# Optimization experiments

Hardware: AMD Instinct MI355X
Metric: run time of the kernel (lower is better)

Reference implementation:

```python
import jax, jax.numpy as jnp
import numpy as np

INF = 1000000000000.0
HEAD_SIZE = 64
HEADS = 12
MAX_LENGTH = 512


def _rope_tables(dim, max_length):
    inv_freq = 1.0 / (10000.0 ** (jnp.arange(0, dim, 2, dtype=jnp.float32) / dim))
    t = jnp.arange(max_length, dtype=jnp.float32)
    freqs = t[:, None] * inv_freq[None, :]  # [L, dim/2]
    return jnp.sin(freqs), jnp.cos(freqs)


def _apply_rope(t, sin, cos):
    # t: [B, L, d]; sin/cos: [L, d/2]
    t1, t2 = t[..., 0::2], t[..., 1::2]
    out = jnp.stack([t1 * cos - t2 * sin, t1 * sin + t2 * cos], axis=-1)
    return out.reshape(t.shape)


def setup_inputs() -> dict:
    key = jax.random.key(0)
    k1, k2, k3, k4, k5 = jax.random.split(key, 5)
    B, L, H = 16, 512, 1024
    inputs = jax.random.normal(k1, (B, L, H), dtype=jnp.float32)
    attention_mask = jnp.ones((B, L), dtype=jnp.float32)
    s1 = 1.0 / np.sqrt(H)
    s2 = 1.0 / np.sqrt(HEAD_SIZE * 2)
    W1 = jax.random.normal(k2, (H, HEAD_SIZE * 2), dtype=jnp.float32) * s1
    b1 = jax.random.normal(k3, (HEAD_SIZE * 2,), dtype=jnp.float32) * s1
    W2 = jax.random.normal(k4, (HEAD_SIZE * 2, HEADS * 2), dtype=jnp.float32) * s2
    b2 = jax.random.normal(k5, (HEADS * 2,), dtype=jnp.float32) * s2
    return {"inputs": inputs, "attention_mask": attention_mask,
            "W1": W1, "b1": b1, "W2": W2, "b2": b2}


def reference(inputs, attention_mask, W1, b1, W2, b2):
    B, L, _ = inputs.shape
    x = inputs @ W1 + b1                      # [B, L, 2*head_size]
    qw, kw = x[..., 0::2], x[..., 1::2]        # [B, L, head_size] each
    sin, cos = _rope_tables(HEAD_SIZE, MAX_LENGTH)
    sin, cos = sin[:L], cos[:L]
    qw = _apply_rope(qw, sin, cos)
    kw = _apply_rope(kw, sin, cos)
    logits = jnp.einsum('bmd,bnd->bmn', qw, kw) / (HEAD_SIZE ** 0.5)  # [B, L, L]
    bias = jnp.swapaxes(x @ W2 + b2, 1, 2) / 2.0                       # [B, 2*heads, L]
    # logits[b,h,m,n] = score[b,m,n] + bias_even[b,h,n] + bias_odd[b,h,m]
    logits = logits[:, None] + bias[:, 0::2, None, :] + bias[:, 1::2, :, None]
    attn_mask = 1.0 - attention_mask[:, None, None, :] * attention_mask[:, None, :, None]
    logits = logits - attn_mask * INF
    tril = jnp.tril(jnp.ones((L, L), dtype=logits.dtype), k=-1)
    logits = logits - tril * INF
    return logits
```

## Files before the change

kernel.cpp:

```cpp
#include <hip/hip_runtime.h>
#include <hip/hip_bf16.h>

typedef short bf16x8 __attribute__((ext_vector_type(8)));
typedef float f32x4 __attribute__((ext_vector_type(4)));
typedef unsigned short u16;
typedef unsigned short u16x4 __attribute__((ext_vector_type(4)));
typedef unsigned short u16x8 __attribute__((ext_vector_type(8)));

#define FINF 1.0e12f

__device__ __forceinline__ u16 f2b(float f) {
  union { float f; unsigned int u; } x; x.f = f;
  unsigned int r = x.u + 0x7fffu + ((x.u >> 16) & 1u);
  return (u16)(r >> 16);
}

__global__ __launch_bounds__(256) void k0_w1frag(const float* __restrict__ W1,
                                                 u16* __restrict__ w1f) {
  int t8 = blockIdx.x * 256 + threadIdx.x;
  int ln = t8 & 15;
  int kg = (t8 >> 4) & 3;
  int ksnt = (t8 >> 6) & 15;
  int chunk = t8 >> 10;
  int ks = ksnt & 1, nt = ksnt >> 1;
  int kbase = chunk * 64 + ks * 32 + kg * 8;
  int c = nt * 16 + ln;
  u16x8 v;
  #pragma unroll
  for (int i = 0; i < 8; ++i) v[i] = f2b(W1[(size_t)(kbase + i) * 128 + c]);
  *(u16x8*)&w1f[t8 * 8] = v;
}

__global__ __launch_bounds__(256) void k1_prep(
    const float* __restrict__ inputs, const u16* __restrict__ w1f,
    const float* __restrict__ b1, const float* __restrict__ W2,
    const float* __restrict__ b2,
    u16* __restrict__ qw, u16* __restrict__ kw,
    float* __restrict__ biasE, float* __restrict__ biasO) {
  __shared__ __align__(16) char smem[49536];
  float* w2t = (float*)(smem + 36864);
  float* xt  = (float*)smem;

  int t = threadIdx.x;
  int lane = t & 63, w = t >> 6;
  int r0 = blockIdx.x * 16;
  int b = r0 >> 9, l0 = r0 & 511;

  #pragma unroll
  for (int i = 0; i < 12; ++i) {
    int idx = t + i * 256;
    int k = idx / 24, c = idx - k * 24;
    w2t[c * 132 + k] = W2[idx];
  }

  f32x4 acc[2];
  acc[0] = (f32x4){0.f, 0.f, 0.f, 0.f};
  acc[1] = (f32x4){0.f, 0.f, 0.f, 0.f};

  int wnt = w * 2;

  int arow_s = t >> 4;
  int aseg = t & 15;
  const float* ain = &inputs[(size_t)(r0 + arow_s) * 1024 + aseg * 4];
  int abyt = (arow_s * 128 + aseg * 8) ^ ((arow_s & 7) << 4);
  const float4* wsrcAll = (const float4*)w1f;

  float4 a0 = *(const float4*)(ain);
  float4 wr0 = wsrcAll[t];
  float4 wr1 = wsrcAll[t + 256];
  float4 wr2 = wsrcAll[t + 512];
  float4 wr3 = wsrcAll[t + 768];
  {
    u16x4 av;
    av[0] = f2b(a0.x); av[1] = f2b(a0.y); av[2] = f2b(a0.z); av[3] = f2b(a0.w);
    *(u16x4*)(smem + abyt) = av;
    float4* wd = (float4*)(smem + 4096);
    wd[t] = wr0; wd[t + 256] = wr1; wd[t + 512] = wr2; wd[t + 768] = wr3;
  }
  __syncthreads();

  for (int ch = 0; ch < 16; ++ch) {
    if (ch < 15) {
      a0 = *(const float4*)(ain + (ch + 1) * 64);
      const float4* wsrc = wsrcAll + (ch + 1) * 1024;
      wr0 = wsrc[t]; wr1 = wsrc[t + 256]; wr2 = wsrc[t + 512]; wr3 = wsrc[t + 768];
    }
    {
      const char* Ab = smem + (ch & 1) * 2048;
      const u16* Wb = (const u16*)(smem + 4096 + (ch & 1) * 16384);
      int arow = lane & 15;
      int hi = lane >> 4;
      #pragma unroll
      for (int ks = 0; ks < 2; ++ks) {
        int cb = ks * 64 + hi * 16;
        bf16x8 a = *(const bf16x8*)(Ab + ((arow * 128 + cb) ^ ((arow & 7) << 4)));
        #pragma unroll
        for (int nti = 0; nti < 2; ++nti) {
          int nt = wnt + nti;
          bf16x8 bb = *(const bf16x8*)&Wb[((nt * 2 + ks) * 64 + lane) * 8];
          acc[nti] = __builtin_amdgcn_mfma_f32_16x16x32_bf16(a, bb, acc[nti], 0, 0, 0);
        }
      }
    }
    if (ch < 15) {
      int q = (ch + 1) & 1;
      u16x4 av;
      av[0] = f2b(a0.x); av[1] = f2b(a0.y); av[2] = f2b(a0.z); av[3] = f2b(a0.w);
      *(u16x4*)(smem + q * 2048 + abyt) = av;
      float4* wd = (float4*)(smem + 4096 + q * 16384);
      wd[t] = wr0; wd[t + 256] = wr1; wd[t + 512] = wr2; wd[t + 768] = wr3;
    }
    __syncthreads();
  }
  __syncthreads();

  #pragma unroll
  for (int nti = 0; nti < 2; ++nti) {
    int c = (wnt + nti) * 16 + (lane & 15);
    float b1v = b1[c];
    #pragma unroll
    for (int r = 0; r < 4; ++r) {
      int row = ((lane >> 4) << 2) + r;
      xt[row * 132 + c] = acc[nti][r] + b1v;
    }
  }
  __syncthreads();

  {
    int r = t >> 4, jb = (t & 15) * 2;
    int l = l0 + r;
    float fl = (float)l;
    u16x4 qv, kv;
    #pragma unroll
    for (int p = 0; p < 2; ++p) {
      int j = jb + p;
      float4 x4 = *(const float4*)&xt[r * 132 + 4 * j];
      float invf = exp2f(-0.4152410118609203f * (float)j);
      float ang = fl * invf;
      float rev = ang * 0.15915494309189535f;
      rev = rev - floorf(rev);
      float sv, cv;
      __sincosf(rev * 6.2831853071795864f, &sv, &cv);
      qv[2 * p] = f2b(x4.x * cv - x4.z * sv);
      qv[2 * p + 1] = f2b(x4.x * sv + x4.z * cv);
      kv[2 * p] = f2b(x4.y * cv - x4.w * sv);
      kv[2 * p + 1] = f2b(x4.y * sv + x4.w * cv);
    }
    size_t base = ((size_t)(b * 512 + l)) * 64 + jb * 2;
    *(u16x4*)&qw[base] = qv;
    *(u16x4*)&kw[base] = kv;
  }

  if (t < 192) {
    int c = t >> 3;
    int rg = (t & 7) * 2;
    float s0 = b2[c], s1 = s0;
    #pragma unroll
    for (int k4 = 0; k4 < 32; ++k4) {
      float4 wv = *(const float4*)&w2t[c * 132 + k4 * 4];
      float4 x0 = *(const float4*)&xt[(rg + 0) * 132 + k4 * 4];
      float4 x1 = *(const float4*)&xt[(rg + 1) * 132 + k4 * 4];
      s0 += x0.x * wv.x + x0.y * wv.y + x0.z * wv.z + x0.w * wv.w;
      s1 += x1.x * wv.x + x1.y * wv.y + x1.z * wv.z + x1.w * wv.w;
    }
    int h = c >> 1;
    size_t o = ((size_t)(b * 12 + h)) * 512 + l0 + rg;
    float2 sv = {s0 * 0.5f, s1 * 0.5f};
    if (c & 1) *(float2*)&biasO[o] = sv;
    else       *(float2*)&biasE[o] = sv;
  }
}

__global__ __launch_bounds__(256) void k2_main(
    const u16* __restrict__ qw, const u16* __restrict__ kw,
    const float* __restrict__ biasE, const float* __restrict__ biasO,
    const float* __restrict__ amask, float* __restrict__ out) {
  __shared__ char smem[24448];
  u16* Q = (u16*)smem;
  u16* K = (u16*)(smem + 8192);
  float* qkL = (float*)smem;
  float* BN = (float*)(smem + 17408);
  float* BM = (float*)(smem + 17408 + 3264);
  float* AMm = (float*)(smem + 17408 + 6528);
  float* AMn = AMm + 64;

  int t = threadIdx.x;
  int lane = t & 63, w = t >> 6;
  int n0 = blockIdx.x * 64, m0 = blockIdx.y * 64, b = blockIdx.z;
  bool skip = (m0 >= n0 + 64);

  if (!skip) {
    int row = t >> 2, sg = t & 3;
    const u16x8* qsrc = (const u16x8*)&qw[((size_t)(b * 512 + m0 + row)) * 64 + sg * 16];
    u16x8 q0 = qsrc[0], q1 = qsrc[1];
    const u16x8* ksrc = (const u16x8*)&kw[((size_t)(b * 512 + n0 + row)) * 64 + sg * 16];
    u16x8 k0v = ksrc[0], k1v = ksrc[1];
    int swz = (row & 7) << 4;
    int byt = row * 128 + sg * 32;
    *(u16x8*)((char*)Q + ((byt) ^ swz)) = q0;
    *(u16x8*)((char*)Q + ((byt + 16) ^ swz)) = q1;
    *(u16x8*)((char*)K + ((byt) ^ swz)) = k0v;
    *(u16x8*)((char*)K + ((byt + 16) ^ swz)) = k1v;
  }
  if (t < 192) {
    int h = t >> 4, kq = t & 15;
    *(float4*)&BN[h * 68 + kq * 4] =
        *(const float4*)&biasE[((size_t)(b * 12 + h)) * 512 + n0 + kq * 4];
    *(float4*)&BM[h * 68 + kq * 4] =
        *(const float4*)&biasO[((size_t)(b * 12 + h)) * 512 + m0 + kq * 4];
  } else if (t < 224) {
    int i = t - 192;
    if (i < 16) *(float4*)&AMm[i * 4] = *(const float4*)&amask[b * 512 + m0 + i * 4];
    else { int ii = i - 16; *(float4*)&AMn[ii * 4] = *(const float4*)&amask[b * 512 + n0 + ii * 4]; }
  }
  __syncthreads();

  if (!skip) {
    f32x4 acc[4];
    #pragma unroll
    for (int nt = 0; nt < 4; ++nt) acc[nt] = (f32x4){0.f, 0.f, 0.f, 0.f};
    int mrow = w * 16 + (lane & 15);
    int hi = lane >> 4;
    #pragma unroll
    for (int ks = 0; ks < 2; ++ks) {
      int cb = ks * 64 + hi * 16;
      bf16x8 a = *(const bf16x8*)((const char*)Q +
                                  ((mrow * 128 + cb) ^ ((mrow & 7) << 4)));
      #pragma unroll
      for (int nt = 0; nt < 4; ++nt) {
        int nr = nt * 16 + (lane & 15);
        bf16x8 bb = *(const bf16x8*)((const char*)K +
                                     ((nr * 128 + cb) ^ ((nr & 7) << 4)));
        acc[nt] = __builtin_amdgcn_mfma_f32_16x16x32_bf16(a, bb, acc[nt], 0, 0, 0);
      }
    }
    __syncthreads();
    #pragma unroll
    for (int nt = 0; nt < 4; ++nt)
      #pragma unroll
      for (int r = 0; r < 4; ++r)
        qkL[(w * 16 + hi * 4 + r) * 68 + nt * 16 + (lane & 15)] = acc[nt][r];
    __syncthreads();
  }

  int a15 = t & 15, mb = t >> 4;
  float amn0 = AMn[a15 * 4 + 0], amn1 = AMn[a15 * 4 + 1];
  float amn2 = AMn[a15 * 4 + 2], amn3 = AMn[a15 * 4 + 3];
  float vals[4][4];
  #pragma unroll
  for (int mi = 0; mi < 4; ++mi) {
    int m = mb + 16 * mi;
    int mg = m0 + m;
    float amm = AMm[m];
    int ng = n0 + a15 * 4;
    float p0 = (1.f - amm * amn0) * FINF + ((mg > ng + 0) ? FINF : 0.f);
    float p1 = (1.f - amm * amn1) * FINF + ((mg > ng + 1) ? FINF : 0.f);
    float p2 = (1.f - amm * amn2) * FINF + ((mg > ng + 2) ? FINF : 0.f);
    float p3 = (1.f - amm * amn3) * FINF + ((mg > ng + 3) ? FINF : 0.f);
    if (!skip) {
      float4 qk = *(const float4*)&qkL[m * 68 + a15 * 4];
      vals[mi][0] = qk.x * 0.125f - p0;
      vals[mi][1] = qk.y * 0.125f - p1;
      vals[mi][2] = qk.z * 0.125f - p2;
      vals[mi][3] = qk.w * 0.125f - p3;
    } else {
      vals[mi][0] = -p0; vals[mi][1] = -p1; vals[mi][2] = -p2; vals[mi][3] = -p3;
    }
  }

  size_t outbase = (size_t)(b * 12) * 262144 + (size_t)m0 * 512 + n0 + a15 * 4;
  #pragma unroll
  for (int h = 0; h < 12; ++h) {
    float4 bn = *(const float4*)&BN[h * 68 + a15 * 4];
    #pragma unroll
    for (int mi = 0; mi < 4; ++mi) {
      int m = mb + 16 * mi;
      float bm = BM[h * 68 + m];
      float4 v;
      v.x = vals[mi][0] + bn.x + bm;
      v.y = vals[mi][1] + bn.y + bm;
      v.z = vals[mi][2] + bn.z + bm;
      v.w = vals[mi][3] + bn.w + bm;
      *(float4*)&out[outbase + (size_t)h * 262144 + (size_t)m * 512] = v;
    }
  }
}

extern "C" void kernel_launch(void* const* d_in, const int* in_sizes, int n_in,
                              void* d_out, int out_size, void* d_ws, size_t ws_size,
                              hipStream_t stream) {
  const float* inputs = (const float*)d_in[0];
  const float* amask  = (const float*)d_in[1];
  const float* W1     = (const float*)d_in[2];
  const float* b1     = (const float*)d_in[3];
  const float* W2     = (const float*)d_in[4];
  const float* b2     = (const float*)d_in[5];
  float* out = (float*)d_out;

  char* ws = (char*)d_ws;
  u16* qw      = (u16*)(ws);
  u16* kw      = (u16*)(ws + (1u << 20));
  float* biasE = (float*)(ws + (2u << 20));
  float* biasO = (float*)(ws + (2u << 20) + 393216u);
  u16* w1f     = (u16*)(ws + (2u << 20) + 786432u);

  k0_w1frag<<<64, 256, 0, stream>>>(W1, w1f);
  k1_prep<<<512, 256, 0, stream>>>(inputs, w1f, b1, W2, b2, qw, kw, biasE, biasO);
  k2_main<<<dim3(8, 8, 16), 256, 0, stream>>>(qw, kw, biasE, biasO, amask, out);
}
```

Before: 56.07 us.

## Fuse three kernels into one persistent kernel with grid-wide atomic barriers

Merges the W1 fragment conversion, the projection/RoPE/bias prep, and the main logits kernel into a single 512-block launch. Device-side atomic-counter barriers separate the phases, and each block handles two output tiles in the last phase. The aim is to remove the launch gaps and tail effects between kernels. In exchange it adds a memset, spin-wait barriers that depend on all 512 blocks being co-resident, and halves parallelism in the output phase.

Measured after the change: 122.0 us. +117.5%, slower.

```diff
diff --git a/kernel.cpp b/kernel.cpp
--- a/kernel.cpp
+++ b/kernel.cpp
@@ -8,6 +8,7 @@
 typedef unsigned short u16x8 __attribute__((ext_vector_type(8)));
 
 #define FINF 1.0e12f
+#define NBLK 512u
 
 __device__ __forceinline__ u16 f2b(float f) {
   union { float f; unsigned int u; } x; x.f = f;
@@ -15,274 +16,289 @@
   return (u16)(r >> 16);
 }
 
-__global__ __launch_bounds__(256) void k0_w1frag(const float* __restrict__ W1,
-                                                 u16* __restrict__ w1f) {
-  int t8 = blockIdx.x * 256 + threadIdx.x;
-  int ln = t8 & 15;
-  int kg = (t8 >> 4) & 3;
-  int ksnt = (t8 >> 6) & 15;
-  int chunk = t8 >> 10;
-  int ks = ksnt & 1, nt = ksnt >> 1;
-  int kbase = chunk * 64 + ks * 32 + kg * 8;
-  int c = nt * 16 + ln;
-  u16x8 v;
-  #pragma unroll
-  for (int i = 0; i < 8; ++i) v[i] = f2b(W1[(size_t)(kbase + i) * 128 + c]);
-  *(u16x8*)&w1f[t8 * 8] = v;
+__device__ __forceinline__ void gbar(unsigned int* cnt) {
+  __syncthreads();
+  if (threadIdx.x == 0) {
+    __threadfence();
+    atomicAdd(cnt, 1u);
+    while (atomicAdd(cnt, 0u) < NBLK) __builtin_amdgcn_s_sleep(8);
+    __threadfence();
+  }
+  __syncthreads();
 }
 
-__global__ __launch_bounds__(256) void k1_prep(
-    const float* __restrict__ inputs, const u16* __restrict__ w1f,
-    const float* __restrict__ b1, const float* __restrict__ W2,
-    const float* __restrict__ b2,
+__global__ __launch_bounds__(256) void fused_all(
+    const float* __restrict__ inputs, const float* __restrict__ amask,
+    const float* __restrict__ W1, const float* __restrict__ b1,
+    const float* __restrict__ W2, const float* __restrict__ b2,
     u16* __restrict__ qw, u16* __restrict__ kw,
-    float* __restrict__ biasE, float* __restrict__ biasO) {
+    float* __restrict__ biasE, float* __restrict__ biasO,
+    u16* __restrict__ w1f, unsigned int* __restrict__ cnt,
+    float* __restrict__ out) {
   __shared__ __align__(16) char smem[49536];
-  float* w2t = (float*)(smem + 36864);
-  float* xt  = (float*)smem;
-
+
+  int bi = blockIdx.x;
   int t = threadIdx.x;
   int lane = t & 63, w = t >> 6;
-  int r0 = blockIdx.x * 16;
-  int b = r0 >> 9, l0 = r0 & 511;
-
-  #pragma unroll
-  for (int i = 0; i < 12; ++i) {
-    int idx = t + i * 256;
-    int k = idx / 24, c = idx - k * 24;
-    w2t[c * 132 + k] = W2[idx];
+
+  if (bi < 64) {
+    int t8 = bi * 256 + t;
+    int ln = t8 & 15;
+    int kg = (t8 >> 4) & 3;
+    int ksnt = (t8 >> 6) & 15;
+    int chunk = t8 >> 10;
+    int ks = ksnt & 1, nt = ksnt >> 1;
+    int kbase = chunk * 64 + ks * 32 + kg * 8;
+    int c = nt * 16 + ln;
+    u16x8 v;
+    #pragma unroll
+    for (int i = 0; i < 8; ++i) v[i] = f2b(W1[(size_t)(kbase + i) * 128 + c]);
+    *(u16x8*)&w1f[t8 * 8] = v;
   }
-
-  f32x4 acc[2];
-  acc[0] = (f32x4){0.f, 0.f, 0.f, 0.f};
-  acc[1] = (f32x4){0.f, 0.f, 0.f, 0.f};
-
-  int wnt = w * 2;
-
-  int arow_s = t >> 4;
-  int aseg = t & 15;
-  const float* ain = &inputs[(size_t)(r0 + arow_s) * 1024 + aseg * 4];
-  int abyt = (arow_s * 128 + aseg * 8) ^ ((arow_s & 7) << 4);
-  const float4* wsrcAll = (const float4*)w1f;
-
-  float4 a0 = *(const float4*)(ain);
-  float4 wr0 = wsrcAll[t];
-  float4 wr1 = wsrcAll[t + 256];
-  float4 wr2 = wsrcAll[t + 512];
-  float4 wr3 = wsrcAll[t + 768];
+  gbar(cnt);
+
   {
-    u16x4 av;
-    av[0] = f2b(a0.x); av[1] = f2b(a0.y); av[2] = f2b(a0.z); av[3] = f2b(a0.w);
-    *(u16x4*)(smem + abyt) = av;
-    float4* wd = (float4*)(smem + 4096);
-    wd[t] = wr0; wd[t + 256] = wr1; wd[t + 512] = wr2; wd[t + 768] = wr3;
+    float* w2t = (float*)(smem + 36864);
+    float* xt  = (float*)smem;
+    int r0 = bi * 16;
+    int b = r0 >> 9, l0 = r0 & 511;
+
+    #pragma unroll
+    for (int i = 0; i < 12; ++i) {
+      int idx = t + i * 256;
+      int k = idx / 24, c = idx - k * 24;
+      w2t[c * 132 + k] = W2[idx];
+    }
+
+    f32x4 acc[2];
+    acc[0] = (f32x4){0.f, 0.f, 0.f, 0.f};
+    acc[1] = (f32x4){0.f, 0.f, 0.f, 0.f};
+
+    int wnt = w * 2;
+
+    int arow_s = t >> 4;
+    int aseg = t & 15;
+    const float* ain = &inputs[(size_t)(r0 + arow_s) * 1024 + aseg * 4];
+    int abyt = (arow_s * 128 + aseg * 8) ^ ((arow_s & 7) << 4);
+    const float4* wsrcAll = (const float4*)w1f;
+
+    float4 a0 = *(const float4*)(ain);
+    float4 wr0 = wsrcAll[t];
+    float4 wr1 = wsrcAll[t + 256];
+    float4 wr2 = wsrcAll[t + 512];
+    float4 wr3 = wsrcAll[t + 768];
+    {
+      u16x4 av;
+      av[0] = f2b(a0.x); av[1] = f2b(a0.y); av[2] = f2b(a0.z); av[3] = f2b(a0.w);
+      *(u16x4*)(smem + abyt) = av;
+      float4* wd = (float4*)(smem + 4096);
+      wd[t] = wr0; wd[t + 256] = wr1; wd[t + 512] = wr2; wd[t + 768] = wr3;
+    }
+    __syncthreads();
+
+    for (int ch = 0; ch < 16; ++ch) {
+      if (ch < 15) {
+        a0 = *(const float4*)(ain + (ch + 1) * 64);
+        const float4* wsrc = wsrcAll + (ch + 1) * 1024;
+        wr0 = wsrc[t]; wr1 = wsrc[t + 256]; wr2 = wsrc[t + 512]; wr3 = wsrc[t + 768];
+      }
+      {
+        const char* Ab = smem + (ch & 1) * 2048;
+        const u16* Wb = (const u16*)(smem + 4096 + (ch & 1) * 16384);
+        int arow = lane & 15;
+        int hi = lane >> 4;
+        #pragma unroll
+        for (int ks = 0; ks < 2; ++ks) {
+          int cb = ks * 64 + hi * 16;
+          bf16x8 a = *(const bf16x8*)(Ab + ((arow * 128 + cb) ^ ((arow & 7) << 4)));
+          #pragma unroll
+          for (int nti = 0; nti < 2; ++nti) {
+            int nt = wnt + nti;
+            bf16x8 bb = *(const bf16x8*)&Wb[((nt * 2 + ks) * 64 + lane) * 8];
+            acc[nti] = __builtin_amdgcn_mfma_f32_16x16x32_bf16(a, bb, acc[nti], 0, 0, 0);
+          }
+        }
+      }
+      if (ch < 15) {
+        int q = (ch + 1) & 1;
+        u16x4 av;
+        av[0] = f2b(a0.x); av[1] = f2b(a0.y); av[2] = f2b(a0.z); av[3] = f2b(a0.w);
+        *(u16x4*)(smem + q * 2048 + abyt) = av;
+        float4* wd = (float4*)(smem + 4096 + q * 16384);
+        wd[t] = wr0; wd[t + 256] = wr1; wd[t + 512] = wr2; wd[t + 768] = wr3;
+      }
+      __syncthreads();
+    }
+    __syncthreads();
+
+    #pragma unroll
+    for (int nti = 0; nti < 2; ++nti) {
+      int c = (wnt + nti) * 16 + (lane & 15);
+      float b1v = b1[c];
+      #pragma unroll
+      for (int r = 0; r < 4; ++r) {
+        int row = ((lane >> 4) << 2) + r;
+        xt[row * 132 + c] = acc[nti][r] + b1v;
+      }
+    }
+    __syncthreads();
+
+    {
+      int r = t >> 4, jb = (t & 15) * 2;
+      int l = l0 + r;
+      float fl = (float)l;
+      u16x4 qv, kv;
+      #pragma unroll
+      for (int p = 0; p < 2; ++p) {
+        int j = jb + p;
+        float4 x4 = *(const float4*)&xt[r * 132 + 4 * j];
+        float invf = exp2f(-0.4152410118609203f * (float)j);
+        float ang = fl * invf;
+        float rev = ang * 0.15915494309189535f;
+        rev = rev - floorf(rev);
+        float sv, cv;
+        __sincosf(rev * 6.2831853071795864f, &sv, &cv);
+        qv[2 * p] = f2b(x4.x * cv - x4.z * sv);
+        qv[2 * p + 1] = f2b(x4.x * sv + x4.z * cv);
+        kv[2 * p] = f2b(x4.y * cv - x4.w * sv);
+        kv[2 * p + 1] = f2b(x4.y * sv + x4.w * cv);
+      }
+      size_t base = ((size_t)(b * 512 + l)) * 64 + jb * 2;
+      *(u16x4*)&qw[base] = qv;
+      *(u16x4*)&kw[base] = kv;
+    }
+
+    if (t < 192) {
+      int c = t >> 3;
+      int rg = (t & 7) * 2;
+      float s0 = b2[c], s1 = s0;
+      #pragma unroll
+      for (int k4 = 0; k4 < 32; ++k4) {
+        float4 wv = *(const float4*)&w2t[c * 132 + k4 * 4];
+        float4 x0 = *(const float4*)&xt[(rg + 0) * 132 + k4 * 4];
+        float4 x1 = *(const float4*)&xt[(rg + 1) * 132 + k4 * 4];
+        s0 += x0.x * wv.x + x0.y * wv.y + x0.z * wv.z + x0.w * wv.w;
+        s1 += x1.x * wv.x + x1.y * wv.y + x1.z * wv.z + x1.w * wv.w;
+      }
+      int h = c >> 1;
+      size_t o = ((size_t)(b * 12 + h)) * 512 + l0 + rg;
+      float2 sv = {s0 * 0.5f, s1 * 0.5f};
+      if (c & 1) *(float2*)&biasO[o] = sv;
+      else       *(float2*)&biasE[o] = sv;
+    }
   }
-  __syncthreads();
-
-  for (int ch = 0; ch < 16; ++ch) {
-    if (ch < 15) {
-      a0 = *(const float4*)(ain + (ch + 1) * 64);
-      const float4* wsrc = wsrcAll + (ch + 1) * 1024;
-      wr0 = wsrc[t]; wr1 = wsrc[t + 256]; wr2 = wsrc[t + 512]; wr3 = wsrc[t + 768];
-    }
-    {
-      const char* Ab = smem + (ch & 1) * 2048;
-      const u16* Wb = (const u16*)(smem + 4096 + (ch & 1) * 16384);
-      int arow = lane & 15;
+  gbar(cnt + 16);
+
+  for (int rep = 0; rep < 2; ++rep) {
+    __syncthreads();
+    u16* Q = (u16*)smem;
+    u16* K = (u16*)(smem + 8192);
+    float* qkL = (float*)smem;
+    float* BN = (float*)(smem + 17408);
+    float* BM = (float*)(smem + 17408 + 3264);
+    float* AMm = (float*)(smem + 17408 + 6528);
+    float* AMn = AMm + 64;
+
+    int tile = bi + rep * 512;
+    int n0 = (tile & 7) * 64, m0 = ((tile >> 3) & 7) * 64, b = tile >> 6;
+    bool skip = (m0 >= n0 + 64);
+
+    if (!skip) {
+      int row = t >> 2, sg = t & 3;
+      const u16x8* qsrc = (const u16x8*)&qw[((size_t)(b * 512 + m0 + row)) * 64 + sg * 16];
+      u16x8 q0 = qsrc[0], q1 = qsrc[1];
+      const u16x8* ksrc = (const u16x8*)&kw[((size_t)(b * 512 + n0 + row)) * 64 + sg * 16];
+      u16x8 k0v = ksrc[0], k1v = ksrc[1];
+      int swz = (row & 7) << 4;
+      int byt = row * 128 + sg * 32;
+      *(u16x8*)((char*)Q + ((byt) ^ swz)) = q0;
+      *(u16x8*)((char*)Q + ((byt + 16) ^ swz)) = q1;
+      *(u16x8*)((char*)K + ((byt) ^ swz)) = k0v;
+      *(u16x8*)((char*)K + ((byt + 16) ^ swz)) = k1v;
+    }
+    if (t < 192) {
+      int h = t >> 4, kq = t & 15;
+      *(float4*)&BN[h * 68 + kq * 4] =
+          *(const float4*)&biasE[((size_t)(b * 12 + h)) * 512 + n0 + kq * 4];
+      *(float4*)&BM[h * 68 + kq * 4] =
+          *(const float4*)&biasO[((size_t)(b * 12 + h)) * 512 + m0 + kq * 4];
+    } else if (t < 224) {
+      int i = t - 192;
+      if (i < 16) *(float4*)&AMm[i * 4] = *(const float4*)&amask[b * 512 + m0 + i * 4];
+      else { int ii = i - 16; *(float4*)&AMn[ii * 4] = *(const float4*)&amask[b * 512 + n0 + ii * 4]; }
+    }
+    __syncthreads();
+
+    if (!skip) {
+      f32x4 acc[4];
+      #pragma unroll
+      for (int nt = 0; nt < 4; ++nt) acc[nt] = (f32x4){0.f, 0.f, 0.f, 0.f};
+      int mrow = w * 16 + (lane & 15);
       int hi = lane >> 4;
       #pragma unroll
       for (int ks = 0; ks < 2; ++ks) {
         int cb = ks * 64 + hi * 16;
-        bf16x8 a = *(const bf16x8*)(Ab + ((arow * 128 + cb) ^ ((arow & 7) << 4)));
+        bf16x8 a = *(const bf16x8*)((const char*)Q +
+                                    ((mrow * 128 + cb) ^ ((mrow & 7) << 4)));
         #pragma unroll
-        for (int nti = 0; nti < 2; ++nti) {
-          int nt = wnt + nti;
-          bf16x8 bb = *(const bf16x8*)&Wb[((nt * 2 + ks) * 64 + lane) * 8];
-          acc[nti] = __builtin_amdgcn_mfma_f32_16x16x32_bf16(a, bb, acc[nti], 0, 0, 0);
+        for (int nt = 0; nt < 4; ++nt) {
+          int nr = nt * 16 + (lane & 15);
+          bf16x8 bb = *(const bf16x8*)((const char*)K +
+                                       ((nr * 128 + cb) ^ ((nr & 7) << 4)));
+          acc[nt] = __builtin_amdgcn_mfma_f32_16x16x32_bf16(a, bb, acc[nt], 0, 0, 0);
         }
       }
-    }
-    if (ch < 15) {
-      int q = (ch + 1) & 1;
-      u16x4 av;
-      av[0] = f2b(a0.x); av[1] = f2b(a0.y); av[2] = f2b(a0.z); av[3] = f2b(a0.w);
-      *(u16x4*)(smem + q * 2048 + abyt) = av;
-      float4* wd = (float4*)(smem + 4096 + q * 16384);
-      wd[t] = wr0; wd[t + 256] = wr1; wd[t + 512] = wr2; wd[t + 768] = wr3;
-    }
-    __syncthreads();
-  }
-  __syncthreads();
-
-  #pragma unroll
-  for (int nti = 0; nti < 2; ++nti) {
-    int c = (wnt + nti) * 16 + (lane & 15);
-    float b1v = b1[c];
-    #pragma unroll
-    for (int r = 0; r < 4; ++r) {
-      int row = ((lane >> 4) << 2) + r;
-      xt[row * 132 + c] = acc[nti][r] + b1v;
-    }
-  }
-  __syncthreads();
-
-  {
-    int r = t >> 4, jb = (t & 15) * 2;
-    int l = l0 + r;
-    float fl = (float)l;
-    u16x4 qv, kv;
-    #pragma unroll
-    for (int p = 0; p < 2; ++p) {
-      int j = jb + p;
-      float4 x4 = *(const float4*)&xt[r * 132 + 4 * j];
-      float invf = exp2f(-0.4152410118609203f * (float)j);
-      float ang = fl * invf;
-      float rev = ang * 0.15915494309189535f;
-      rev = rev - floorf(rev);
-      float sv, cv;
-      __sincosf(rev * 6.2831853071795864f, &sv, &cv);
-      qv[2 * p] = f2b(x4.x * cv - x4.z * sv);
-      qv[2 * p + 1] = f2b(x4.x * sv + x4.z * cv);
-      kv[2 * p] = f2b(x4.y * cv - x4.w * sv);
-      kv[2 * p + 1] = f2b(x4.y * sv + x4.w * cv);
-    }
-    size_t base = ((size_t)(b * 512 + l)) * 64 + jb * 2;
-    *(u16x4*)&qw[base] = qv;
-    *(u16x4*)&kw[base] = kv;
-  }
-
-  if (t < 192) {
-    int c = t >> 3;
-    int rg = (t & 7) * 2;
-    float s0 = b2[c], s1 = s0;
-    #pragma unroll
-    for (int k4 = 0; k4 < 32; ++k4) {
-      float4 wv = *(const float4*)&w2t[c * 132 + k4 * 4];
-      float4 x0 = *(const float4*)&xt[(rg + 0) * 132 + k4 * 4];
-      float4 x1 = *(const float4*)&xt[(rg + 1) * 132 + k4 * 4];
-      s0 += x0.x * wv.x + x0.y * wv.y + x0.z * wv.z + x0.w * wv.w;
-      s1 += x1.x * wv.x + x1.y * wv.y + x1.z * wv.z + x1.w * wv.w;
-    }
-    int h = c >> 1;
-    size_t o = ((size_t)(b * 12 + h)) * 512 + l0 + rg;
-    float2 sv = {s0 * 0.5f, s1 * 0.5f};
-    if (c & 1) *(float2*)&biasO[o] = sv;
-    else       *(float2*)&biasE[o] = sv;
-  }
-}
-
-__global__ __launch_bounds__(256) void k2_main(
-    const u16* __restrict__ qw, const u16* __restrict__ kw,
-    const float* __restrict__ biasE, const float* __restrict__ biasO,
-    const float* __restrict__ amask, float* __restrict__ out) {
-  __shared__ char smem[24448];
-  u16* Q = (u16*)smem;
-  u16* K = (u16*)(smem + 8192);
-  float* qkL = (float*)smem;
-  float* BN = (float*)(smem + 17408);
-  float* BM = (float*)(smem + 17408 + 3264);
-  float* AMm = (float*)(smem + 17408 + 6528);
-  float* AMn = AMm + 64;
-
-  int t = threadIdx.x;
-  int lane = t & 63, w = t >> 6;
-  int n0 = blockIdx.x * 64, m0 = blockIdx.y * 64, b = blockIdx.z;
-  bool skip = (m0 >= n0 + 64);
-
-  if (!skip) {
-    int row = t >> 2, sg = t & 3;
-    const u16x8* qsrc = (const u16x8*)&qw[((size_t)(b * 512 + m0 + row)) * 64 + sg * 16];
-    u16x8 q0 = qsrc[0], q1 = qsrc[1];
-    const u16x8* ksrc = (const u16x8*)&kw[((size_t)(b * 512 + n0 + row)) * 64 + sg * 16];
-    u16x8 k0v = ksrc[0], k1v = ksrc[1];
-    int swz = (row & 7) << 4;
-    int byt = row * 128 + sg * 32;
-    *(u16x8*)((char*)Q + ((byt) ^ swz)) = q0;
-    *(u16x8*)((char*)Q + ((byt + 16) ^ swz)) = q1;
-    *(u16x8*)((char*)K + ((byt) ^ swz)) = k0v;
-    *(u16x8*)((char*)K + ((byt + 16) ^ swz)) = k1v;
-  }
-  if (t < 192) {
-    int h = t >> 4, kq = t & 15;
-    *(float4*)&BN[h * 68 + kq * 4] =
-        *(const float4*)&biasE[((size_t)(b * 12 + h)) * 512 + n0 + kq * 4];
-    *(float4*)&BM[h * 68 + kq * 4] =
-        *(const float4*)&biasO[((size_t)(b * 12 + h)) * 512 + m0 + kq * 4];
-  } else if (t < 224) {
-    int i = t - 192;
-    if (i < 16) *(float4*)&AMm[i * 4] = *(const float4*)&amask[b * 512 + m0 + i * 4];
-    else { int ii = i - 16; *(float4*)&AMn[ii * 4] = *(const float4*)&amask[b * 512 + n0 + ii * 4]; }
-  }
-  __syncthreads();
-
-  if (!skip) {
-    f32x4 acc[4];
-    #pragma unroll
-    for (int nt = 0; nt < 4; ++nt) acc[nt] = (f32x4){0.f, 0.f, 0.f, 0.f};
-    int mrow = w * 16 + (lane & 15);
-    int hi = lane >> 4;
-    #pragma unroll
-    for (int ks = 0; ks < 2; ++ks) {
-      int cb = ks * 64 + hi * 16;
-      bf16x8 a = *(const bf16x8*)((const char*)Q +
-                                  ((mrow * 128 + cb) ^ ((mrow & 7) << 4)));
-      #pragma unroll
-      for (int nt = 0; nt < 4; ++nt) {
-        int nr = nt * 16 + (lane & 15);
-        bf16x8 bb = *(const bf16x8*)((const char*)K +
-                                     ((nr * 128 + cb) ^ ((nr & 7) << 4)));
-        acc[nt] = __builtin_amdgcn_mfma_f32_16x16x32_bf16(a, bb, acc[nt], 0, 0, 0);
-      }
-    }
-    __syncthreads();
-    #pragma unroll
-    for (int nt = 0; nt < 4; ++nt)
-      #pragma unroll
-      for (int r = 0; r < 4; ++r)
-        qkL[(w * 16 + hi * 4 + r) * 68 + nt * 16 + (lane & 15)] = acc[nt][r];
-    __syncthreads();
-  }
-
-  int a15 = t & 15, mb = t >> 4;
-  float amn0 = AMn[a15 * 4 + 0], amn1 = AMn[a15 * 4 + 1];
-  float amn2 = AMn[a15 * 4 + 2], amn3 = AMn[a15 * 4 + 3];
-  float vals[4][4];
-  #pragma unroll
-  for (int mi = 0; mi < 4; ++mi) {
-    int m = mb + 16 * mi;
-    int mg = m0 + m;
-    float amm = AMm[m];
-    int ng = n0 + a15 * 4;
-    float p0 = (1.f - amm * amn0) * FINF + ((mg > ng + 0) ? FINF : 0.f);
-    float p1 = (1.f - amm * amn1) * FINF + ((mg > ng + 1) ? FINF : 0.f);
-    float p2 = (1.f - amm * amn2) * FINF + ((mg > ng + 2) ? FINF : 0.f);
-    float p3 = (1.f - amm * amn3) * FINF + ((mg > ng + 3) ? FINF : 0.f);
-    if (!skip) {
-      float4 qk = *(const float4*)&qkL[m * 68 + a15 * 4];
-      vals[mi][0] = qk.x * 0.125f - p0;
-      vals[mi][1] = qk.y * 0.125f - p1;
-      vals[mi][2] = qk.z * 0.125f - p2;
-      vals[mi][3] = qk.w * 0.125f - p3;
-    } else {
-      vals[mi][0] = -p0; vals[mi][1] = -p1; vals[mi][2] = -p2; vals[mi][3] = -p3;
-    }
-  }
-
-  size_t outbase = (size_t)(b * 12) * 262144 + (size_t)m0 * 512 + n0 + a15 * 4;
-  #pragma unroll
-  for (int h = 0; h < 12; ++h) {
-    float4 bn = *(const float4*)&BN[h * 68 + a15 * 4];
+      __syncthreads();
+      #pragma unroll
+      for (int nt = 0; nt < 4; ++nt)
+        #pragma unroll
+        for (int r = 0; r < 4; ++r)
+          qkL[(w * 16 + hi * 4 + r) * 68 + nt * 16 + (lane & 15)] = acc[nt][r];
+      __syncthreads();
+    }
+
+    int a15 = t & 15, mb = t >> 4;
+    float amn0 = AMn[a15 * 4 + 0], amn1 = AMn[a15 * 4 + 1];
+    float amn2 = AMn[a15 * 4 + 2], amn3 = AMn[a15 * 4 + 3];
+    float vals[4][4];
     #pragma unroll
     for (int mi = 0; mi < 4; ++mi) {
       int m = mb + 16 * mi;
-      float bm = BM[h * 68 + m];
-      float4 v;
-      v.x = vals[mi][0] + bn.x + bm;
-      v.y = vals[mi][1] + bn.y + bm;
-      v.z = vals[mi][2] + bn.z + bm;
-      v.w = vals[mi][3] + bn.w + bm;
-      *(float4*)&out[outbase + (size_t)h * 262144 + (size_t)m * 512] = v;
-    }
+      int mg = m0 + m;
+      float amm = AMm[m];
+      int ng = n0 + a15 * 4;
+      float p0 = (1.f - amm * amn0) * FINF + ((mg > ng + 0) ? FINF : 0.f);
+      float p1 = (1.f - amm * amn1) * FINF + ((mg > ng + 1) ? FINF : 0.f);
+      float p2 = (1.f - amm * amn2) * FINF + ((mg > ng + 2) ? FINF : 0.f);
+      float p3 = (1.f - amm * amn3) * FINF + ((mg > ng + 3) ? FINF : 0.f);
+      if (!skip) {
+        float4 qk = *(const float4*)&qkL[m * 68 + a15 * 4];
+        vals[mi][0] = qk.x * 0.125f - p0;
+        vals[mi][1] = qk.y * 0.125f - p1;
+        vals[mi][2] = qk.z * 0.125f - p2;
+        vals[mi][3] = qk.w * 0.125f - p3;
+      } else {
+        vals[mi][0] = -p0; vals[mi][1] = -p1; vals[mi][2] = -p2; vals[mi][3] = -p3;
+      }
+    }
+
+    size_t outbase = (size_t)(b * 12) * 262144 + (size_t)m0 * 512 + n0 + a15 * 4;
+    #pragma unroll
+    for (int h = 0; h < 12; ++h) {
+      float4 bn = *(const float4*)&BN[h * 68 + a15 * 4];
+      #pragma unroll
+      for (int mi = 0; mi < 4; ++mi) {
+        int m = mb + 16 * mi;
+        float bm = BM[h * 68 + m];
+        float4 v;
+        v.x = vals[mi][0] + bn.x + bm;
+        v.y = vals[mi][1] + bn.y + bm;
+        v.z = vals[mi][2] + bn.z + bm;
+        v.w = vals[mi][3] + bn.w + bm;
+        *(float4*)&out[outbase + (size_t)h * 262144 + (size_t)m * 512] = v;
+      }
+    }
+    __syncthreads();
   }
 }
 
@@ -303,8 +319,9 @@
   float* biasE = (float*)(ws + (2u << 20));
   float* biasO = (float*)(ws + (2u << 20) + 393216u);
   u16* w1f     = (u16*)(ws + (2u << 20) + 786432u);
-
-  k0_w1frag<<<64, 256, 0, stream>>>(W1, w1f);
-  k1_prep<<<512, 256, 0, stream>>>(inputs, w1f, b1, W2, b2, qw, kw, biasE, biasO);
-  k2_main<<<dim3(8, 8, 16), 256, 0, stream>>>(qw, kw, biasE, biasO, amask, out);
+  unsigned int* cnt = (unsigned int*)(ws + (2u << 20) + 786432u + 262144u);
+
+  hipMemsetAsync(cnt, 0, 128, stream);
+  fused_all<<<512, 256, 0, stream>>>(inputs, amask, W1, b1, W2, b2, qw, kw,
+                                     biasE, biasO, w1f, cnt, out);
 }
```
